# Kernel optimization log

Measured on AMD Instinct MI355X. Metric: run time of the kernel, lower is better.

## Reference

```python
import jax, jax.numpy as jnp
import numpy as np

N = 100000
E = 1600000
F_IN = 64
ACT = 8
NEG_SLOPE = 0.2


def _p(key, shape, scale=0.1):
    return jax.random.normal(key, shape, dtype=jnp.float32) * scale


def setup_inputs() -> dict:
    key = jax.random.key(0)
    ks = jax.random.split(key, 20)
    x = jax.random.normal(ks[0], (N, F_IN), dtype=jnp.float32)
    edge_index = jax.random.randint(ks[1], (2, E), 0, N, dtype=jnp.int64)
    edge_attr = jax.random.normal(ks[2], (E, 2), dtype=jnp.float32)
    # conv1: in=64, heads=4, out=16 -> 64
    H1, C1 = 4, 16
    Wl1 = _p(ks[3], (F_IN, H1 * C1)); bl1 = jnp.zeros((H1 * C1,), jnp.float32)
    Wr1 = _p(ks[4], (F_IN, H1 * C1)); br1 = jnp.zeros((H1 * C1,), jnp.float32)
    We1 = _p(ks[5], (2, H1 * C1))
    att1 = _p(ks[6], (H1, C1))
    b1 = jnp.zeros((H1 * C1,), jnp.float32)
    # conv2: in=64, heads=2, out=32 -> 64
    H2, C2 = 2, 32
    Wl2 = _p(ks[7], (H1 * C1, H2 * C2)); bl2 = jnp.zeros((H2 * C2,), jnp.float32)
    Wr2 = _p(ks[8], (H1 * C1, H2 * C2)); br2 = jnp.zeros((H2 * C2,), jnp.float32)
    We2 = _p(ks[9], (2, H2 * C2))
    att2 = _p(ks[10], (H2, C2))
    b2 = jnp.zeros((H2 * C2,), jnp.float32)
    Wm = _p(ks[11], (H2 * C2, ACT)); bm = jnp.zeros((ACT,), jnp.float32)
    return dict(x=x, edge_index=edge_index, edge_attr=edge_attr,
                Wl1=Wl1, bl1=bl1, Wr1=Wr1, br1=br1, We1=We1, att1=att1, b1=b1,
                Wl2=Wl2, bl2=bl2, Wr2=Wr2, br2=br2, We2=We2, att2=att2, b2=b2,
                Wm=Wm, bm=bm)


def gatv2_layer(x, src, dst, ea, Wl, bl, Wr, br, We, att, b, n_nodes, heads, ch):
    """PyG GATv2Conv with concat=True, add_self_loops=True (fill_value='mean')."""
    # self loops: edge attr = mean of incoming edge attrs per node (0 if none)
    deg = jax.ops.segment_sum(jnp.ones((src.shape[0],), ea.dtype), dst, n_nodes)
    loop_attr = jax.ops.segment_sum(ea, dst, n_nodes) / jnp.maximum(deg, 1.0)[:, None]
    loop = jnp.arange(n_nodes, dtype=src.dtype)
    s = jnp.concatenate([src, loop]); d = jnp.concatenate([dst, loop])
    ea_full = jnp.concatenate([ea, loop_attr], axis=0)
    xl = (x @ Wl + bl).reshape(n_nodes, heads, ch)   # source transform
    xr = (x @ Wr + br).reshape(n_nodes, heads, ch)   # target transform
    ee = (ea_full @ We).reshape(-1, heads, ch)
    e = jax.nn.leaky_relu(xl[s] + xr[d] + ee, NEG_SLOPE)  # [E', H, C]
    logits = jnp.einsum('ehc,hc->eh', e, att)             # [E', H]
    # segment softmax over destination (every node has a self loop -> non-empty)
    m = jax.ops.segment_max(logits, d, n_nodes)
    expl = jnp.exp(logits - m[d])
    denom = jax.ops.segment_sum(expl, d, n_nodes)
    alpha = expl / (denom[d] + 1e-16)
    out = jax.ops.segment_sum(xl[s] * alpha[:, :, None], d, n_nodes)
    return out.reshape(n_nodes, heads * ch) + b


def reference(x, edge_index, edge_attr, Wl1, bl1, Wr1, br1, We1, att1, b1,
              Wl2, bl2, Wr2, br2, We2, att2, b2, Wm, bm):
    src, dst = edge_index[0], edge_index[1]
    h = jax.nn.relu(gatv2_layer(x, src, dst, edge_attr, Wl1, bl1, Wr1, br1,
                                We1, att1, b1, N, 4, 16))
    h = jax.nn.relu(gatv2_layer(h, src, dst, edge_attr, Wl2, bl2, Wr2, br2,
                                We2, att2, b2, N, 2, 32))
    return jnp.tanh(h @ Wm + bm)
```

## Files before the change

kernel.cpp:

```cpp
#include <hip/hip_runtime.h>
#include <hip/hip_bf16.h>


constexpr int CAP = 64;

typedef float v2f __attribute__((ext_vector_type(2)));

static __device__ __forceinline__ float bf2f(__hip_bfloat16 v) { return __bfloat162float(v); }
static __device__ __forceinline__ float bits2f(unsigned int u) { return __uint_as_float(u << 16); }
static __device__ __forceinline__ unsigned int f2bfbits(float f) {
  unsigned int u = __float_as_uint(f);
  return ((u + 0x7FFFu + ((u >> 16) & 1u)) >> 16) & 0xFFFFu;
}
static __device__ __forceinline__ float bcast(float v, int k) {
  return __int_as_float(__builtin_amdgcn_readlane(__float_as_int(v), k));
}

template <int CTRL>
static __device__ __forceinline__ float dpp_add(float v) {
  int m = __builtin_amdgcn_update_dpp(0, __float_as_int(v), CTRL, 0xf, 0xf, false);
  return v + __int_as_float(m);
}
static __device__ __forceinline__ float row16_sum(float p) {
  p = dpp_add<0x128>(p);
  p = dpp_add<0x124>(p);
  p = dpp_add<0x122>(p);
  p = dpp_add<0x121>(p);
  return p;
}
static __device__ __forceinline__ float quad_sum(float p) {
  p = dpp_add<0xB1>(p);
  p = dpp_add<0x4E>(p);
  return p;
}
static __device__ __forceinline__ float wave64_sum(float p) {
  p = row16_sum(p);
  p += __shfl_xor(p, 16);
  p += __shfl_xor(p, 32);
  return p;
}

template <typename T> static __device__ __forceinline__ float ldv(const T* p, size_t i);
template <> __device__ __forceinline__ float ldv<float>(const float* p, size_t i) { return p[i]; }
template <> __device__ __forceinline__ float ldv<__hip_bfloat16>(const __hip_bfloat16* p, size_t i) {
  return bf2f(p[i]);
}
template <typename T> static __device__ __forceinline__ void stv(T* p, size_t i, float v);
template <> __device__ __forceinline__ void stv<float>(float* p, size_t i, float v) { p[i] = v; }
template <> __device__ __forceinline__ void stv<__hip_bfloat16>(__hip_bfloat16* p, size_t i,
                                                                float v) {
  p[i] = __float2bfloat16(v);
}

__global__ void k_count(const int* __restrict__ dst, int* __restrict__ cnt, int E, int N) {
  int i = blockIdx.x * 256 + threadIdx.x;
  if (i >= E) return;
  int d = dst[i]; d = min(max(d, 0), N - 1);
  atomicAdd(&cnt[d], 1);
}

__global__ __launch_bounds__(1024) void k_scan_local(const int* __restrict__ deg,
                                                     int* __restrict__ off,
                                                     int* __restrict__ bsum, int n) {
  __shared__ int s[1024];
  int t = threadIdx.x;
  int g = blockIdx.x * 1024 + t;
  int v = (g < n) ? deg[g] : 0;
  s[t] = v;
  __syncthreads();
  for (int o = 1; o < 1024; o <<= 1) {
    int add = (t >= o) ? s[t - o] : 0;
    __syncthreads();
    s[t] += add;
    __syncthreads();
  }
  if (g < n) off[g] = s[t] - v;
  if (t == 1023) bsum[blockIdx.x] = s[t];
}

__global__ __launch_bounds__(256) void k_scan_part(const int* __restrict__ bsum,
                                                   int* __restrict__ boff,
                                                   int* __restrict__ off, int nb, int n) {
  __shared__ int s[256];
  int t = threadIdx.x;
  int v = (t < nb) ? bsum[t] : 0;
  s[t] = v;
  __syncthreads();
  for (int o = 1; o < 256; o <<= 1) {
    int add = (t >= o) ? s[t - o] : 0;
    __syncthreads();
    s[t] += add;
    __syncthreads();
  }
  if (t < nb) boff[t] = s[t] - v;
  if (t == nb - 1) off[n] = s[t];
}

__global__ __launch_bounds__(1024) void k_scan_add(int* __restrict__ off, int* __restrict__ cursor,
                                                   const int* __restrict__ boff, int n) {
  int g = blockIdx.x * 1024 + threadIdx.x;
  if (g < n) {
    int v = off[g] + boff[blockIdx.x];
    off[g] = v;
    cursor[g] = v;
  }
}

__global__ void k_scatter_x(const int* __restrict__ src, const int* __restrict__ dst,
                            const float* __restrict__ ea, int* __restrict__ cursor,
                            long long* __restrict__ csr, int E, int N) {
  const int group = blockIdx.x & 7;
  const int chunk = blockIdx.x >> 3;
  const int r0 = (int)(((long long)N * group) >> 3);
  const int r1 = (int)(((long long)N * (group + 1)) >> 3);
  int i0 = (chunk * 256 + threadIdx.x) * 4;
  if (i0 >= E) return;
  if (i0 + 4 <= E) {
    int4 sv = *(const int4*)(src + i0);
    int4 dv = *(const int4*)(dst + i0);
    float4 ea01 = *(const float4*)(ea + 2 * i0);
    float4 ea23 = *(const float4*)(ea + 2 * i0 + 4);
    int ss[4] = {sv.x, sv.y, sv.z, sv.w};
    int dd[4] = {dv.x, dv.y, dv.z, dv.w};
    float e0[4] = {ea01.x, ea01.z, ea23.x, ea23.z};
    float e1[4] = {ea01.y, ea01.w, ea23.y, ea23.w};
#pragma unroll
    for (int j = 0; j < 4; ++j) {
      int d = min(max(dd[j], 0), N - 1);
      if (d >= r0 && d < r1) {
        int s = min(max(ss[j], 0), N - 1);
        unsigned int ep = f2bfbits(e0[j]) | (f2bfbits(e1[j]) << 16);
        long long rec = (long long)(unsigned int)s | ((long long)ep << 32);
        int slot = atomicAdd(&cursor[d], 1);
        if (slot < CAP) csr[(long long)d * CAP + slot] = rec;
      }
    }
  } else {
    for (int i = i0; i < E; ++i) {
      int d = min(max(dst[i], 0), N - 1);
      if (d >= r0 && d < r1) {
        int s = min(max(src[i], 0), N - 1);
        unsigned int ep = f2bfbits(ea[2 * i]) | (f2bfbits(ea[2 * i + 1]) << 16);
        long long rec = (long long)(unsigned int)s | ((long long)ep << 32);
        int slot = atomicAdd(&cursor[d], 1);
        if (slot < CAP) csr[(long long)d * CAP + slot] = rec;
      }
    }
  }
}

__global__ void k_scatter_d(const int* __restrict__ src, const int* __restrict__ dst,
                            const float* __restrict__ ea, int* __restrict__ cursor,
                            long long* __restrict__ csr, int E, int N) {
  int i = blockIdx.x * 256 + threadIdx.x;
  if (i >= E) return;
  int d = min(max(dst[i], 0), N - 1);
  int s = min(max(src[i], 0), N - 1);
  unsigned int ep = f2bfbits(ea[2 * i]) | (f2bfbits(ea[2 * i + 1]) << 16);
  long long rec = (long long)(unsigned int)s | ((long long)ep << 32);
  int slot = atomicAdd(&cursor[d], 1);
  csr[slot] = rec;
}

__global__ __launch_bounds__(256) void k_gemm_xlxr(const float* __restrict__ in,
                                                   const float* __restrict__ Wl,
                                                   const float* __restrict__ bl,
                                                   const float* __restrict__ Wr,
                                                   const float* __restrict__ br,
                                                   unsigned short* __restrict__ xlb,
                                                   float* __restrict__ xr, int n) {
  int lane = threadIdx.x & 63, wave = threadIdx.x >> 6;
  float wl[64], wr[64];
#pragma unroll
  for (int k = 0; k < 64; ++k) {
    wl[k] = Wl[k * 64 + lane];
    wr[k] = Wr[k * 64 + lane];
  }
  float blc = bl[lane], brc = br[lane];
  const int stride = gridDim.x * 4;
  int node = blockIdx.x * 4 + wave;
  if (node >= n) return;
  float xv = in[(size_t)node * 64 + lane];
  while (node < n) {
    int nxt = node + stride;
    float xn = (nxt < n) ? in[(size_t)nxt * 64 + lane] : 0.f;
    float accl = blc, accr = brc;
#pragma unroll
    for (int k = 0; k < 64; ++k) {
      float s = bcast(xv, k);
      accl = fmaf(s, wl[k], accl);
      accr = fmaf(s, wr[k], accr);
    }
    xlb[(size_t)node * 64 + lane] = (unsigned short)f2bfbits(accl);
    xr[(size_t)node * 64 + lane] = accr;
    node = nxt;
    xv = xn;
  }
}

template <int C, bool FUSE_MLP>
__global__ __launch_bounds__(256) void k_agg4p(const unsigned short* __restrict__ xlb,
                                               const float* __restrict__ xr,
                                               const long long* __restrict__ csr,
                                               const int* __restrict__ cnt,
                                               const float* __restrict__ We,
                                               const float* __restrict__ att,
                                               const float* __restrict__ b,
                                               const float* __restrict__ Wm,
                                               const float* __restrict__ bm,
                                               float* __restrict__ hout,
                                               float* __restrict__ fout, int n) {
  __shared__ long long smeta[4][CAP];
  const int lane = threadIdx.x & 63;
  const int wv = threadIdx.x >> 6;
  const int sub = lane & 15;
  const int grp = lane >> 4;

  float4 t4;
  t4 = ((const float4*)We)[sub];        const v2f We0a = {t4.x, t4.y}, We0b = {t4.z, t4.w};
  t4 = ((const float4*)(We + 64))[sub]; const v2f We1a = {t4.x, t4.y}, We1b = {t4.z, t4.w};
  t4 = ((const float4*)att)[sub];       const v2f atta = {t4.x, t4.y}, attb = {t4.z, t4.w};
  t4 = ((const float4*)b)[sub];         const v2f ba = {t4.x, t4.y},  bb = {t4.z, t4.w};

  const int wstride = gridDim.x * 4;
  for (int wid = blockIdx.x * 4 + wv; wid < n; wid += wstride) {
    const int node = __builtin_amdgcn_readfirstlane(wid);
    float4 x4 = ((const float4*)(xr + (size_t)node * 64))[sub];
    const v2f xra = {x4.x, x4.y}, xrb = {x4.z, x4.w};
    uint2 xself = ((const uint2*)xlb)[((unsigned)node << 4) + sub];

    int dg = cnt[node];
    int c64 = min(dg, CAP);
    long long meta = (lane < c64) ? __builtin_nontemporal_load(&csr[(size_t)node * CAP + lane])
                                  : 0LL;
    smeta[wv][lane] = meta;
    int mhi = (int)((unsigned long long)meta >> 32);
    float ea0acc = __uint_as_float((unsigned)mhi << 16);
    float ea1acc = __uint_as_float((unsigned)mhi & 0xffff0000u);

    float den = 0.f;
    v2f numa = {0.f, 0.f}, numb = {0.f, 0.f};

    int iters = (c64 + 3) >> 2;
    long long m0 = smeta[wv][grp];
    uint2 xg0 = ((const uint2*)xlb)[(((unsigned)(unsigned int)m0) << 4) + sub];
    for (int t = 0; t < iters; ++t) {
      long long m1 = 0;
      uint2 xg1 = {0u, 0u};
      if (t + 1 < iters) {
        m1 = smeta[wv][(t + 1) * 4 + grp];
        xg1 = ((const uint2*)xlb)[(((unsigned)(unsigned int)m1) << 4) + sub];
      }
      unsigned epc = (unsigned)((unsigned long long)m0 >> 32);
      float ea0 = __uint_as_float(epc << 16);
      float ea1 = __uint_as_float(epc & 0xffff0000u);
      v2f ea0v = {ea0, ea0}, ea1v = {ea1, ea1};
      v2f xca = {__uint_as_float(xg0.x << 16), __uint_as_float(xg0.x & 0xffff0000u)};
      v2f xcb = {__uint_as_float(xg0.y << 16), __uint_as_float(xg0.y & 0xffff0000u)};
      v2f eA = __builtin_elementwise_fma(We1a, ea1v,
               __builtin_elementwise_fma(We0a, ea0v, xca + xra));
      v2f eB = __builtin_elementwise_fma(We1b, ea1v,
               __builtin_elementwise_fma(We0b, ea0v, xcb + xrb));
      eA = __builtin_elementwise_max(eA, eA * 0.2f);
      eB = __builtin_elementwise_max(eB, eB * 0.2f);
      v2f pv = __builtin_elementwise_fma(eB, attb, eA * atta);
      float p = pv.x + pv.y;
      p = quad_sum(p);
      if (C == 32) p = dpp_add<0x141>(p);
      bool valid = ((t << 2) + grp) < c64;
      float ex = valid ? __expf(p) : 0.f;
      v2f exv = {ex, ex};
      den += ex;
      numa = __builtin_elementwise_fma(exv, xca, numa);
      numb = __builtin_elementwise_fma(exv, xcb, numb);
      m0 = m1;
      xg0 = xg1;
    }

    den += __shfl_xor(den, 16);
    den += __shfl_xor(den, 32);
    numa.x += __shfl_xor(numa.x, 16); numa.x += __shfl_xor(numa.x, 32);
    numa.y += __shfl_xor(numa.y, 16); numa.y += __shfl_xor(numa.y, 32);
    numb.x += __shfl_xor(numb.x, 16); numb.x += __shfl_xor(numb.x, 32);
    numb.y += __shfl_xor(numb.y, 16); numb.y += __shfl_xor(numb.y, 32);

    v2f xsa = {__uint_as_float(xself.x << 16), __uint_as_float(xself.x & 0xffff0000u)};
    v2f xsb = {__uint_as_float(xself.y << 16), __uint_as_float(xself.y & 0xffff0000u)};
    {
      float s0 = wave64_sum(ea0acc);
      float s1 = wave64_sum(ea1acc);
      float inv = 1.0f / (float)max(dg, 1);
      v2f a0v = {s0 * inv, s0 * inv}, a1v = {s1 * inv, s1 * inv};
      v2f eA = __builtin_elementwise_fma(We1a, a1v,
               __builtin_elementwise_fma(We0a, a0v, xsa + xra));
      v2f eB = __builtin_elementwise_fma(We1b, a1v,
               __builtin_elementwise_fma(We0b, a0v, xsb + xrb));
      eA = __builtin_elementwise_max(eA, eA * 0.2f);
      eB = __builtin_elementwise_max(eB, eB * 0.2f);
      v2f pv = __builtin_elementwise_fma(eB, attb, eA * atta);
      float p = quad_sum(pv.x + pv.y);
      if (C == 32) p = dpp_add<0x141>(p);
      float ex = __expf(p);
      v2f exv = {ex, ex};
      den += ex;
      numa = __builtin_elementwise_fma(exv, xsa, numa);
      numb = __builtin_elementwise_fma(exv, xsb, numb);
    }

    float inv = 1.0f / (den + 1e-16f);
    v2f invv = {inv, inv};
    v2f oa = __builtin_elementwise_max(__builtin_elementwise_fma(numa, invv, ba), (v2f){0.f, 0.f});
    v2f ob = __builtin_elementwise_max(__builtin_elementwise_fma(numb, invv, bb), (v2f){0.f, 0.f});

    if (!FUSE_MLP) {
      if (grp == 0) {
        float4 o4 = {oa.x, oa.y, ob.x, ob.y};
        ((float4*)(hout + (size_t)node * 64))[sub] = o4;
      }
    } else {
      float mine = 0.f;
#pragma unroll
      for (int j = 0; j < 8; ++j) {
        float p = oa.x * Wm[(4 * sub + 0) * 8 + j];
        p = fmaf(oa.y, Wm[(4 * sub + 1) * 8 + j], p);
        p = fmaf(ob.x, Wm[(4 * sub + 2) * 8 + j], p);
        p = fmaf(ob.y, Wm[(4 * sub + 3) * 8 + j], p);
        p = row16_sum(p);
        if (lane == j) mine = p;
      }
      if (lane < 8) fout[(size_t)node * 8 + lane] = tanhf(mine + bm[lane]);
    }
  }
}

template <int C, bool FUSE_MLP>
__global__ __launch_bounds__(256) void k_agg4d(const unsigned short* __restrict__ xlb,
                                               const float* __restrict__ xr,
                                               const long long* __restrict__ csr,
                                               const int* __restrict__ off,
                                               const float* __restrict__ We,
                                               const float* __restrict__ att,
                                               const float* __restrict__ b,
                                               const float* __restrict__ Wm,
                                               const float* __restrict__ bm,
                                               float* __restrict__ hout,
                                               float* __restrict__ fout, int n) {
  const int lane = threadIdx.x & 63;
  const int sub = lane & 15;
  const int grp = lane >> 4;
  const int grp4 = grp << 2;
  const float4 We04 = ((const float4*)We)[sub];
  const float4 We14 = ((const float4*)(We + 64))[sub];
  const float4 att4 = ((const float4*)att)[sub];
  const float4 b4 = ((const float4*)b)[sub];

  const int wstride = gridDim.x * 4;
  for (int wid = blockIdx.x * 4 + (threadIdx.x >> 6); wid < n; wid += wstride) {
    const int node = __builtin_amdgcn_readfirstlane(wid);
    float4 xr4 = ((const float4*)(xr + (size_t)node * 64))[sub];
    uint2 xself = ((const uint2*)xlb)[((unsigned)node << 4) + sub];
    int start = off[node], end = off[node + 1], dg = end - start;
    float den = 0.f;
    float4 num = {0.f, 0.f, 0.f, 0.f};
    float ea0acc = 0.f, ea1acc = 0.f;
    for (int base = start; base < end; base += 64) {
      int c64 = min(64, end - base);
      long long meta = (lane < c64) ? __builtin_nontemporal_load(&csr[base + lane]) : 0LL;
      int mlo = (int)(unsigned long long)meta;
      int mhi = (int)((unsigned long long)meta >> 32);
      ea0acc += __uint_as_float((unsigned)mhi << 16);
      ea1acc += __uint_as_float((unsigned)mhi & 0xffff0000u);
      int iters = (c64 + 3) >> 2;
      int se0 = __builtin_amdgcn_ds_bpermute(grp4, mlo);
      int ep0 = __builtin_amdgcn_ds_bpermute(grp4, mhi);
      uint2 xg0 = ((const uint2*)xlb)[((unsigned)se0 << 4) + sub];
      for (int t = 0; t < iters; ++t) {
        int ep1 = 0;
        uint2 xg1 = {0u, 0u};
        if (t + 1 < iters) {
          int idx = ((t + 1) << 4) + grp4;
          int se1 = __builtin_amdgcn_ds_bpermute(idx, mlo);
          ep1 = __builtin_amdgcn_ds_bpermute(idx, mhi);
          xg1 = ((const uint2*)xlb)[((unsigned)se1 << 4) + sub];
        }
        float4 xc;
        xc.x = __uint_as_float(xg0.x << 16);
        xc.y = __uint_as_float(xg0.x & 0xffff0000u);
        xc.z = __uint_as_float(xg0.y << 16);
        xc.w = __uint_as_float(xg0.y & 0xffff0000u);
        unsigned epc = (unsigned)ep0;
        float ea0 = __uint_as_float(epc << 16);
        float ea1 = __uint_as_float(epc & 0xffff0000u);
        float4 e;
        e.x = fmaf(ea1, We14.x, fmaf(ea0, We04.x, xc.x + xr4.x));
        e.y = fmaf(ea1, We14.y, fmaf(ea0, We04.y, xc.y + xr4.y));
        e.z = fmaf(ea1, We14.z, fmaf(ea0, We04.z, xc.z + xr4.z));
        e.w = fmaf(ea1, We14.w, fmaf(ea0, We04.w, xc.w + xr4.w));
        e.x = fmaxf(e.x, 0.2f * e.x);
        e.y = fmaxf(e.y, 0.2f * e.y);
        e.z = fmaxf(e.z, 0.2f * e.z);
        e.w = fmaxf(e.w, 0.2f * e.w);
        float p = e.x * att4.x;
        p = fmaf(e.y, att4.y, p);
        p = fmaf(e.z, att4.z, p);
        p = fmaf(e.w, att4.w, p);
        p = quad_sum(p);
        if (C == 32) p = dpp_add<0x141>(p);
        bool valid = ((t << 2) + grp) < c64;
        float ex = valid ? __expf(p) : 0.f;
        den += ex;
        num.x = fmaf(ex, xc.x, num.x);
        num.y = fmaf(ex, xc.y, num.y);
        num.z = fmaf(ex, xc.z, num.z);
        num.w = fmaf(ex, xc.w, num.w);
        ep0 = ep1;
        xg0 = xg1;
      }
    }
    den += __shfl_xor(den, 16);
    den += __shfl_xor(den, 32);
    num.x += __shfl_xor(num.x, 16); num.x += __shfl_xor(num.x, 32);
    num.y += __shfl_xor(num.y, 16); num.y += __shfl_xor(num.y, 32);
    num.z += __shfl_xor(num.z, 16); num.z += __shfl_xor(num.z, 32);
    num.w += __shfl_xor(num.w, 16); num.w += __shfl_xor(num.w, 32);
    float4 xls4;
    xls4.x = __uint_as_float(xself.x << 16);
    xls4.y = __uint_as_float(xself.x & 0xffff0000u);
    xls4.z = __uint_as_float(xself.y << 16);
    xls4.w = __uint_as_float(xself.y & 0xffff0000u);
    {
      float s0 = wave64_sum(ea0acc);
      float s1 = wave64_sum(ea1acc);
      float inv = 1.0f / (float)max(dg, 1);
      float a0 = s0 * inv, a1 = s1 * inv;
      float4 e;
      e.x = fmaf(a1, We14.x, fmaf(a0, We04.x, xls4.x + xr4.x));
      e.y = fmaf(a1, We14.y, fmaf(a0, We04.y, xls4.y + xr4.y));
      e.z = fmaf(a1, We14.z, fmaf(a0, We04.z, xls4.z + xr4.z));
      e.w = fmaf(a1, We14.w, fmaf(a0, We04.w, xls4.w + xr4.w));
      e.x = fmaxf(e.x, 0.2f * e.x);
      e.y = fmaxf(e.y, 0.2f * e.y);
      e.z = fmaxf(e.z, 0.2f * e.z);
      e.w = fmaxf(e.w, 0.2f * e.w);
      float p = e.x * att4.x;
      p = fmaf(e.y, att4.y, p);
      p = fmaf(e.z, att4.z, p);
      p = fmaf(e.w, att4.w, p);
      p = quad_sum(p);
      if (C == 32) p = dpp_add<0x141>(p);
      float ex = __expf(p);
      den += ex;
      num.x = fmaf(ex, xls4.x, num.x);
      num.y = fmaf(ex, xls4.y, num.y);
      num.z = fmaf(ex, xls4.z, num.z);
      num.w = fmaf(ex, xls4.w, num.w);
    }
    float inv = 1.0f / (den + 1e-16f);
    float4 o;
    o.x = fmaxf(fmaf(num.x, inv, b4.x), 0.f);
    o.y = fmaxf(fmaf(num.y, inv, b4.y), 0.f);
    o.z = fmaxf(fmaf(num.z, inv, b4.z), 0.f);
    o.w = fmaxf(fmaf(num.w, inv, b4.w), 0.f);
    if (!FUSE_MLP) {
      if (grp == 0) ((float4*)(hout + (size_t)node * 64))[sub] = o;
    } else {
      float mine = 0.f;
#pragma unroll
      for (int j = 0; j < 8; ++j) {
        float p = o.x * Wm[(4 * sub + 0) * 8 + j];
        p = fmaf(o.y, Wm[(4 * sub + 1) * 8 + j], p);
        p = fmaf(o.z, Wm[(4 * sub + 2) * 8 + j], p);
        p = fmaf(o.w, Wm[(4 * sub + 3) * 8 + j], p);
        p = row16_sum(p);
        if (lane == j) mine = p;
      }
      if (lane < 8) fout[(size_t)node * 8 + lane] = tanhf(mine + bm[lane]);
    }
  }
}

template <typename TIN, typename TOUT>
__global__ __launch_bounds__(256) void k_gemm_gen(const TIN* __restrict__ in,
                                                  const float* __restrict__ Wl,
                                                  const float* __restrict__ bl,
                                                  const float* __restrict__ Wr,
                                                  const float* __restrict__ br,
                                                  TOUT* __restrict__ xl, TOUT* __restrict__ xr,
                                                  int n) {
  int lane = threadIdx.x & 63, wave = threadIdx.x >> 6;
  float wl[64], wr[64];
#pragma unroll
  for (int k = 0; k < 64; ++k) {
    wl[k] = Wl[k * 64 + lane];
    wr[k] = Wr[k * 64 + lane];
  }
  float blc = bl[lane], brc = br[lane];
  for (int node = blockIdx.x * 4 + wave; node < n; node += gridDim.x * 4) {
    float xv = ldv(in, (size_t)node * 64 + lane);
    float accl = blc, accr = brc;
#pragma unroll
    for (int k = 0; k < 64; ++k) {
      float s = bcast(xv, k);
      accl = fmaf(s, wl[k], accl);
      accr = fmaf(s, wr[k], accr);
    }
    stv(xl, (size_t)node * 64 + lane, accl);
    stv(xr, (size_t)node * 64 + lane, accr);
  }
}

template <int C, bool FUSE_MLP, typename ST>
__global__ __launch_bounds__(256) void k_agg(const ST* __restrict__ xl, const ST* __restrict__ xr,
                                             const long long* __restrict__ csr,
                                             const int* __restrict__ off,
                                             const float* __restrict__ We,
                                             const float* __restrict__ att,
                                             const float* __restrict__ b,
                                             const float* __restrict__ Wm,
                                             const float* __restrict__ bm, ST* __restrict__ hout,
                                             float* __restrict__ fout, int n) {
  int wid = (int)((blockIdx.x * blockDim.x + threadIdx.x) >> 6);
  int lane = threadIdx.x & 63;
  if (wid >= n) return;
  const int node = __builtin_amdgcn_readfirstlane(wid);
  float xr_c = ldv(xr, (size_t)node * 64 + lane);
  float xl_self = ldv(xl, (size_t)node * 64 + lane);
  float We0 = We[lane], We1 = We[64 + lane], attc = att[lane], bc = b[lane];
  int start = off[node], end = off[node + 1], dg = end - start;
  float den = 0.f, num = 0.f, ea0acc = 0.f, ea1acc = 0.f;
  for (int base = start; base < end; base += 64) {
    int c64 = min(64, end - base);
    long long meta = (lane < c64) ? csr[base + lane] : 0;
    int mlo = (int)(unsigned long long)meta;
    int mhi = (int)((unsigned long long)meta >> 32);
    ea0acc += bits2f((unsigned)mhi & 0xffffu);
    ea1acc += bits2f((unsigned)mhi >> 16);
    for (int t = 0; t < c64; ++t) {
      int s = __builtin_amdgcn_readlane(mlo, t);
      unsigned ep = (unsigned)__builtin_amdgcn_readlane(mhi, t);
      float xls = ldv(xl, (size_t)s * 64 + lane);
      float e = xls + xr_c + bits2f(ep & 0xffffu) * We0 + bits2f(ep >> 16) * We1;
      e = fmaxf(e, 0.2f * e);
      float p = row16_sum(e * attc);
      if (C == 32) p += __shfl_xor(p, 16);
      float ex = __expf(p);
      den += ex;
      num = fmaf(ex, xls, num);
    }
  }
  {
    float s0 = wave64_sum(ea0acc), s1 = wave64_sum(ea1acc);
    float inv = 1.0f / (float)max(dg, 1);
    float e = xl_self + xr_c + s0 * inv * We0 + s1 * inv * We1;
    e = fmaxf(e, 0.2f * e);
    float p = row16_sum(e * attc);
    if (C == 32) p += __shfl_xor(p, 16);
    float ex = __expf(p);
    den += ex;
    num = fmaf(ex, xl_self, num);
  }
  float o = fmaxf(num / (den + 1e-16f) + bc, 0.f);
  if (!FUSE_MLP) {
    stv(hout, (size_t)node * 64 + lane, o);
  } else {
    float mine = 0.f;
#pragma unroll
    for (int j = 0; j < 8; ++j) {
      float p = wave64_sum(o * Wm[lane * 8 + j]);
      if (lane == j) mine = p;
    }
    if (lane < 8) fout[(size_t)node * 8 + lane] = tanhf(mine + bm[lane]);
  }
}

extern "C" void kernel_launch(void* const* d_in, const int* in_sizes, int n_in,
                              void* d_out, int out_size, void* d_ws, size_t ws_size,
                              hipStream_t stream) {
  const float* x = (const float*)d_in[0];
  const int* ei = (const int*)d_in[1];
  const float* ea = (const float*)d_in[2];
  const float* Wl1 = (const float*)d_in[3];
  const float* bl1 = (const float*)d_in[4];
  const float* Wr1 = (const float*)d_in[5];
  const float* br1 = (const float*)d_in[6];
  const float* We1 = (const float*)d_in[7];
  const float* att1 = (const float*)d_in[8];
  const float* b1 = (const float*)d_in[9];
  const float* Wl2 = (const float*)d_in[10];
  const float* bl2 = (const float*)d_in[11];
  const float* Wr2 = (const float*)d_in[12];
  const float* br2 = (const float*)d_in[13];
  const float* We2 = (const float*)d_in[14];
  const float* att2 = (const float*)d_in[15];
  const float* b2 = (const float*)d_in[16];
  const float* Wm = (const float*)d_in[17];
  const float* bm = (const float*)d_in[18];
  float* out = (float*)d_out;

  const int N = in_sizes[0] / 64;
  const int E = in_sizes[1] / 2;
  const int* src = ei;
  const int* dst = ei + E;

  auto al = [](size_t x) { return (x + 255) & ~(size_t)255; };
  const size_t needA = al((size_t)N * 4) + al((size_t)N * CAP * 8) + al((size_t)N * 64 * 2) +
                       al((size_t)N * 64 * 4) + al((size_t)N * 64 * 4);
  const size_t fixedB = al((size_t)N * 4) + al((size_t)(N + 1) * 4) + al((size_t)N * 4) +
                        al(1024) + al(1024) + al((size_t)E * 8);
  const size_t needB = fixedB + al((size_t)N * 64 * 2) + 2 * al((size_t)N * 64 * 4);

  char* p = (char*)d_ws;
  auto alloc = [&](size_t bytes) {
    char* r = p;
    p += (bytes + 255) & ~(size_t)255;
    return r;
  };

  const int egrid4 = (E + 1023) / 1024;
  const int egrid = (E + 255) / 256;
  const int agrid = 2048;
  const int ggrid = 1024;
  const int NB = (N + 1023) / 1024;

  if (ws_size >= needA) {
    int* cnt = (int*)alloc((size_t)N * 4);
    long long* csr = (long long*)alloc((size_t)N * CAP * 8);
    unsigned short* xlb = (unsigned short*)alloc((size_t)N * 64 * 2);
    float* xr = (float*)alloc((size_t)N * 64 * 4);
    float* h = (float*)alloc((size_t)N * 64 * 4);

    hipMemsetAsync(cnt, 0, (size_t)N * 4, stream);
    k_scatter_x<<<egrid4 * 8, 256, 0, stream>>>(src, dst, ea, cnt, csr, E, N);

    k_gemm_xlxr<<<ggrid, 256, 0, stream>>>(x, Wl1, bl1, Wr1, br1, xlb, xr, N);
    k_agg4p<16, false><<<agrid, 256, 0, stream>>>(xlb, xr, csr, cnt, We1, att1, b1, nullptr,
                                                  nullptr, h, nullptr, N);
    k_gemm_xlxr<<<ggrid, 256, 0, stream>>>(h, Wl2, bl2, Wr2, br2, xlb, xr, N);
    k_agg4p<32, true><<<agrid, 256, 0, stream>>>(xlb, xr, csr, cnt, We2, att2, b2, Wm, bm,
                                                 nullptr, out, N);
  } else if (ws_size >= needB) {
    int* cnt = (int*)alloc((size_t)N * 4);
    int* off = (int*)alloc((size_t)(N + 1) * 4);
    int* cursor = (int*)alloc((size_t)N * 4);
    int* bsum = (int*)alloc(1024);
    int* boff = (int*)alloc(1024);
    long long* csr = (long long*)alloc((size_t)E * 8);
    unsigned short* xlb = (unsigned short*)alloc((size_t)N * 64 * 2);
    float* xr = (float*)alloc((size_t)N * 64 * 4);
    float* h = (float*)alloc((size_t)N * 64 * 4);

    hipMemsetAsync(cnt, 0, (size_t)N * 4, stream);
    k_count<<<egrid, 256, 0, stream>>>(dst, cnt, E, N);
    k_scan_local<<<NB, 1024, 0, stream>>>(cnt, off, bsum, N);
    k_scan_part<<<1, 256, 0, stream>>>(bsum, boff, off, NB, N);
    k_scan_add<<<NB, 1024, 0, stream>>>(off, cursor, boff, N);
    k_scatter_d<<<egrid, 256, 0, stream>>>(src, dst, ea, cursor, csr, E, N);

    k_gemm_xlxr<<<ggrid, 256, 0, stream>>>(x, Wl1, bl1, Wr1, br1, xlb, xr, N);
    k_agg4d<16, false><<<agrid, 256, 0, stream>>>(xlb, xr, csr, off, We1, att1, b1, nullptr,
                                                  nullptr, h, nullptr, N);
    k_gemm_xlxr<<<ggrid, 256, 0, stream>>>(h, Wl2, bl2, Wr2, br2, xlb, xr, N);
    k_agg4d<32, true><<<agrid, 256, 0, stream>>>(xlb, xr, csr, off, We2, att2, b2, Wm, bm,
                                                 nullptr, out, N);
  } else {
    int* cnt = (int*)alloc((size_t)N * 4);
    int* off = (int*)alloc((size_t)(N + 1) * 4);
    int* cursor = (int*)alloc((size_t)N * 4);
    int* bsum = (int*)alloc(1024);
    int* boff = (int*)alloc(1024);
    long long* csr = (long long*)alloc((size_t)E * 8);
    __hip_bfloat16* xl = (__hip_bfloat16*)alloc((size_t)N * 64 * 2);
    __hip_bfloat16* xr = (__hip_bfloat16*)alloc((size_t)N * 64 * 2);
    __hip_bfloat16* h = (__hip_bfloat16*)alloc((size_t)N * 64 * 2);

    hipMemsetAsync(cnt, 0, (size_t)N * 4, stream);
    k_count<<<egrid, 256, 0, stream>>>(dst, cnt, E, N);
    k_scan_local<<<NB, 1024, 0, stream>>>(cnt, off, bsum, N);
    k_scan_part<<<1, 256, 0, stream>>>(bsum, boff, off, NB, N);
    k_scan_add<<<NB, 1024, 0, stream>>>(off, cursor, boff, N);
    k_scatter_d<<<egrid, 256, 0, stream>>>(src, dst, ea, cursor, csr, E, N);

    k_gemm_gen<float, __hip_bfloat16><<<ggrid, 256, 0, stream>>>(x, Wl1, bl1, Wr1, br1, xl, xr, N);
    k_agg<16, false, __hip_bfloat16><<<(N + 3) / 4, 256, 0, stream>>>(
        xl, xr, csr, off, We1, att1, b1, nullptr, nullptr, h, nullptr, N);
    k_gemm_gen<__hip_bfloat16, __hip_bfloat16><<<ggrid, 256, 0, stream>>>(h, Wl2, bl2, Wr2, br2,
                                                                          xl, xr, N);
    k_agg<32, true, __hip_bfloat16><<<(N + 3) / 4, 256, 0, stream>>>(
        xl, xr, csr, off, We2, att2, b2, Wm, bm, nullptr, out, N);
  }
}
```

Baseline: 450.9 us.

## Process eight edges per wave iteration in GATv2 aggregation with 8-lane groups

Reworks the aggregation kernel so each wave handles eight neighbor edges per iteration instead of four. Each edge is covered by 8 lanes loading 16-byte bf16 chunks rather than 16 lanes loading 8 bytes, which halves the loop trip count and widens the gather loads. Head reductions move to smaller DPP patterns, and the cross-group reductions and the fused MLP are adapted to the new lane layout. In exchange each lane holds more registers and does more arithmetic, and low-degree nodes leave more lanes idle.

After: 470.7 us. +4.4%, slower.

```diff
diff --git a/kernel.cpp b/kernel.cpp
--- a/kernel.cpp
+++ b/kernel.cpp
@@ -28,16 +28,38 @@
   p = dpp_add<0x121>(p);
   return p;
 }
-static __device__ __forceinline__ float quad_sum(float p) {
-  p = dpp_add<0xB1>(p);
-  p = dpp_add<0x4E>(p);
-  return p;
-}
 static __device__ __forceinline__ float wave64_sum(float p) {
   p = row16_sum(p);
   p += __shfl_xor(p, 16);
   p += __shfl_xor(p, 32);
   return p;
+}
+static __device__ __forceinline__ float grp_sum(float v) {
+  v = dpp_add<0x128>(v);
+  v += __shfl_xor(v, 16);
+  v += __shfl_xor(v, 32);
+  return v;
+}
+static __device__ __forceinline__ float sub8_sum(float v) {
+  v = dpp_add<0x124>(v);
+  v = dpp_add<0x122>(v);
+  v = dpp_add<0x121>(v);
+  return v;
+}
+
+static __device__ __forceinline__ void unpack8(uint4 g, v2f* r) {
+  r[0] = (v2f){__uint_as_float(g.x << 16), __uint_as_float(g.x & 0xffff0000u)};
+  r[1] = (v2f){__uint_as_float(g.y << 16), __uint_as_float(g.y & 0xffff0000u)};
+  r[2] = (v2f){__uint_as_float(g.z << 16), __uint_as_float(g.z & 0xffff0000u)};
+  r[3] = (v2f){__uint_as_float(g.w << 16), __uint_as_float(g.w & 0xffff0000u)};
+}
+static __device__ __forceinline__ void load8(const float* p, int sub, v2f* r) {
+  float4 u = ((const float4*)p)[2 * sub];
+  float4 v = ((const float4*)p)[2 * sub + 1];
+  r[0] = (v2f){u.x, u.y};
+  r[1] = (v2f){u.z, u.w};
+  r[2] = (v2f){v.x, v.y};
+  r[3] = (v2f){v.z, v.w};
 }
 
 template <typename T> static __device__ __forceinline__ float ldv(const T* p, size_t i);
@@ -199,7 +221,7 @@
 }
 
 template <int C, bool FUSE_MLP>
-__global__ __launch_bounds__(256) void k_agg4p(const unsigned short* __restrict__ xlb,
+__global__ __launch_bounds__(256) void k_agg8p(const unsigned short* __restrict__ xlb,
                                                const float* __restrict__ xr,
                                                const long long* __restrict__ csr,
                                                const int* __restrict__ cnt,
@@ -213,21 +235,20 @@
   __shared__ long long smeta[4][CAP];
   const int lane = threadIdx.x & 63;
   const int wv = threadIdx.x >> 6;
-  const int sub = lane & 15;
-  const int grp = lane >> 4;
-
-  float4 t4;
-  t4 = ((const float4*)We)[sub];        const v2f We0a = {t4.x, t4.y}, We0b = {t4.z, t4.w};
-  t4 = ((const float4*)(We + 64))[sub]; const v2f We1a = {t4.x, t4.y}, We1b = {t4.z, t4.w};
-  t4 = ((const float4*)att)[sub];       const v2f atta = {t4.x, t4.y}, attb = {t4.z, t4.w};
-  t4 = ((const float4*)b)[sub];         const v2f ba = {t4.x, t4.y},  bb = {t4.z, t4.w};
+  const int sub = lane & 7;
+  const int grp = lane >> 3;
+
+  v2f We0[4], We1[4], attv[4];
+  load8(We, sub, We0);
+  load8(We + 64, sub, We1);
+  load8(att, sub, attv);
 
   const int wstride = gridDim.x * 4;
   for (int wid = blockIdx.x * 4 + wv; wid < n; wid += wstride) {
     const int node = __builtin_amdgcn_readfirstlane(wid);
-    float4 x4 = ((const float4*)(xr + (size_t)node * 64))[sub];
-    const v2f xra = {x4.x, x4.y}, xrb = {x4.z, x4.w};
-    uint2 xself = ((const uint2*)xlb)[((unsigned)node << 4) + sub];
+    v2f xrv[4];
+    load8(xr + (size_t)node * 64, sub, xrv);
+    uint4 xself = ((const uint4*)xlb)[((unsigned)node << 3) + sub];
 
     int dg = cnt[node];
     int c64 = min(dg, CAP);
@@ -239,93 +260,103 @@
     float ea1acc = __uint_as_float((unsigned)mhi & 0xffff0000u);
 
     float den = 0.f;
-    v2f numa = {0.f, 0.f}, numb = {0.f, 0.f};
-
-    int iters = (c64 + 3) >> 2;
+    v2f num[4] = {{0.f, 0.f}, {0.f, 0.f}, {0.f, 0.f}, {0.f, 0.f}};
+
+    int iters = (c64 + 7) >> 3;
     long long m0 = smeta[wv][grp];
-    uint2 xg0 = ((const uint2*)xlb)[(((unsigned)(unsigned int)m0) << 4) + sub];
+    uint4 xg0 = ((const uint4*)xlb)[(((unsigned)(unsigned int)m0) << 3) + sub];
     for (int t = 0; t < iters; ++t) {
       long long m1 = 0;
-      uint2 xg1 = {0u, 0u};
+      uint4 xg1 = {0u, 0u, 0u, 0u};
       if (t + 1 < iters) {
-        m1 = smeta[wv][(t + 1) * 4 + grp];
-        xg1 = ((const uint2*)xlb)[(((unsigned)(unsigned int)m1) << 4) + sub];
+        m1 = smeta[wv][(t + 1) * 8 + grp];
+        xg1 = ((const uint4*)xlb)[(((unsigned)(unsigned int)m1) << 3) + sub];
       }
       unsigned epc = (unsigned)((unsigned long long)m0 >> 32);
-      float ea0 = __uint_as_float(epc << 16);
-      float ea1 = __uint_as_float(epc & 0xffff0000u);
-      v2f ea0v = {ea0, ea0}, ea1v = {ea1, ea1};
-      v2f xca = {__uint_as_float(xg0.x << 16), __uint_as_float(xg0.x & 0xffff0000u)};
-      v2f xcb = {__uint_as_float(xg0.y << 16), __uint_as_float(xg0.y & 0xffff0000u)};
-      v2f eA = __builtin_elementwise_fma(We1a, ea1v,
-               __builtin_elementwise_fma(We0a, ea0v, xca + xra));
-      v2f eB = __builtin_elementwise_fma(We1b, ea1v,
-               __builtin_elementwise_fma(We0b, ea0v, xcb + xrb));
-      eA = __builtin_elementwise_max(eA, eA * 0.2f);
-      eB = __builtin_elementwise_max(eB, eB * 0.2f);
-      v2f pv = __builtin_elementwise_fma(eB, attb, eA * atta);
+      v2f ea0v = {__uint_as_float(epc << 16), __uint_as_float(epc << 16)};
+      v2f ea1v = {__uint_as_float(epc & 0xffff0000u), __uint_as_float(epc & 0xffff0000u)};
+      v2f xc[4];
+      unpack8(xg0, xc);
+      v2f pv;
+#pragma unroll
+      for (int q = 0; q < 4; ++q) {
+        v2f e = __builtin_elementwise_fma(We1[q], ea1v,
+                __builtin_elementwise_fma(We0[q], ea0v, xc[q] + xrv[q]));
+        e = __builtin_elementwise_max(e, e * 0.2f);
+        pv = (q == 0) ? e * attv[0] : __builtin_elementwise_fma(e, attv[q], pv);
+      }
       float p = pv.x + pv.y;
-      p = quad_sum(p);
-      if (C == 32) p = dpp_add<0x141>(p);
-      bool valid = ((t << 2) + grp) < c64;
+      p = dpp_add<0xB1>(p);
+      if (C == 32) p = dpp_add<0x4E>(p);
+      bool valid = (t * 8 + grp) < c64;
       float ex = valid ? __expf(p) : 0.f;
       v2f exv = {ex, ex};
       den += ex;
-      numa = __builtin_elementwise_fma(exv, xca, numa);
-      numb = __builtin_elementwise_fma(exv, xcb, numb);
+#pragma unroll
+      for (int q = 0; q < 4; ++q) num[q] = __builtin_elementwise_fma(exv, xc[q], num[q]);
       m0 = m1;
       xg0 = xg1;
     }
 
-    den += __shfl_xor(den, 16);
-    den += __shfl_xor(den, 32);
-    numa.x += __shfl_xor(numa.x, 16); numa.x += __shfl_xor(numa.x, 32);
-    numa.y += __shfl_xor(numa.y, 16); numa.y += __shfl_xor(numa.y, 32);
-    numb.x += __shfl_xor(numb.x, 16); numb.x += __shfl_xor(numb.x, 32);
-    numb.y += __shfl_xor(numb.y, 16); numb.y += __shfl_xor(numb.y, 32);
-
-    v2f xsa = {__uint_as_float(xself.x << 16), __uint_as_float(xself.x & 0xffff0000u)};
-    v2f xsb = {__uint_as_float(xself.y << 16), __uint_as_float(xself.y & 0xffff0000u)};
+    den = grp_sum(den);
+#pragma unroll
+    for (int q = 0; q < 4; ++q) {
+      num[q].x = grp_sum(num[q].x);
+      num[q].y = grp_sum(num[q].y);
+    }
+
+    v2f xs[4];
+    unpack8(xself, xs);
     {
       float s0 = wave64_sum(ea0acc);
       float s1 = wave64_sum(ea1acc);
-      float inv = 1.0f / (float)max(dg, 1);
-      v2f a0v = {s0 * inv, s0 * inv}, a1v = {s1 * inv, s1 * inv};
-      v2f eA = __builtin_elementwise_fma(We1a, a1v,
-               __builtin_elementwise_fma(We0a, a0v, xsa + xra));
-      v2f eB = __builtin_elementwise_fma(We1b, a1v,
-               __builtin_elementwise_fma(We0b, a0v, xsb + xrb));
-      eA = __builtin_elementwise_max(eA, eA * 0.2f);
-      eB = __builtin_elementwise_max(eB, eB * 0.2f);
-      v2f pv = __builtin_elementwise_fma(eB, attb, eA * atta);
-      float p = quad_sum(pv.x + pv.y);
-      if (C == 32) p = dpp_add<0x141>(p);
+      float minv = 1.0f / (float)max(dg, 1);
+      v2f a0v = {s0 * minv, s0 * minv}, a1v = {s1 * minv, s1 * minv};
+      v2f pv;
+#pragma unroll
+      for (int q = 0; q < 4; ++q) {
+        v2f e = __builtin_elementwise_fma(We1[q], a1v,
+                __builtin_elementwise_fma(We0[q], a0v, xs[q] + xrv[q]));
+        e = __builtin_elementwise_max(e, e * 0.2f);
+        pv = (q == 0) ? e * attv[0] : __builtin_elementwise_fma(e, attv[q], pv);
+      }
+      float p = pv.x + pv.y;
+      p = dpp_add<0xB1>(p);
+      if (C == 32) p = dpp_add<0x4E>(p);
       float ex = __expf(p);
       v2f exv = {ex, ex};
       den += ex;
-      numa = __builtin_elementwise_fma(exv, xsa, numa);
-      numb = __builtin_elementwise_fma(exv, xsb, numb);
-    }
-
-    float inv = 1.0f / (den + 1e-16f);
-    v2f invv = {inv, inv};
-    v2f oa = __builtin_elementwise_max(__builtin_elementwise_fma(numa, invv, ba), (v2f){0.f, 0.f});
-    v2f ob = __builtin_elementwise_max(__builtin_elementwise_fma(numb, invv, bb), (v2f){0.f, 0.f});
+#pragma unroll
+      for (int q = 0; q < 4; ++q) num[q] = __builtin_elementwise_fma(exv, xs[q], num[q]);
+    }
+
+    float invd = 1.0f / (den + 1e-16f);
+    v2f invv = {invd, invd};
+    v2f bv[4];
+    load8(b, sub, bv);
+    v2f o[4];
+#pragma unroll
+    for (int q = 0; q < 4; ++q)
+      o[q] = __builtin_elementwise_max(__builtin_elementwise_fma(num[q], invv, bv[q]),
+                                       (v2f){0.f, 0.f});
 
     if (!FUSE_MLP) {
       if (grp == 0) {
-        float4 o4 = {oa.x, oa.y, ob.x, ob.y};
-        ((float4*)(hout + (size_t)node * 64))[sub] = o4;
+        float4 oA = {o[0].x, o[0].y, o[1].x, o[1].y};
+        float4 oB = {o[2].x, o[2].y, o[3].x, o[3].y};
+        ((float4*)(hout + (size_t)node * 64))[2 * sub] = oA;
+        ((float4*)(hout + (size_t)node * 64))[2 * sub + 1] = oB;
       }
     } else {
+      const float* wmrow = Wm + (8 * sub) * 8;
+      float oc[8] = {o[0].x, o[0].y, o[1].x, o[1].y, o[2].x, o[2].y, o[3].x, o[3].y};
       float mine = 0.f;
 #pragma unroll
       for (int j = 0; j < 8; ++j) {
-        float p = oa.x * Wm[(4 * sub + 0) * 8 + j];
-        p = fmaf(oa.y, Wm[(4 * sub + 1) * 8 + j], p);
-        p = fmaf(ob.x, Wm[(4 * sub + 2) * 8 + j], p);
-        p = fmaf(ob.y, Wm[(4 * sub + 3) * 8 + j], p);
-        p = row16_sum(p);
+        float p = oc[0] * wmrow[j];
+#pragma unroll
+        for (int k = 1; k < 8; ++k) p = fmaf(oc[k], wmrow[k * 8 + j], p);
+        p = sub8_sum(p);
         if (lane == j) mine = p;
       }
       if (lane < 8) fout[(size_t)node * 8 + lane] = tanhf(mine + bm[lane]);
@@ -404,7 +435,8 @@
         p = fmaf(e.y, att4.y, p);
         p = fmaf(e.z, att4.z, p);
         p = fmaf(e.w, att4.w, p);
-        p = quad_sum(p);
+        p = dpp_add<0xB1>(p);
+        p = dpp_add<0x4E>(p);
         if (C == 32) p = dpp_add<0x141>(p);
         bool valid = ((t << 2) + grp) < c64;
         float ex = valid ? __expf(p) : 0.f;
@@ -446,7 +478,8 @@
       p = fmaf(e.y, att4.y, p);
       p = fmaf(e.z, att4.z, p);
       p = fmaf(e.w, att4.w, p);
-      p = quad_sum(p);
+      p = dpp_add<0xB1>(p);
+      p = dpp_add<0x4E>(p);
       if (C == 32) p = dpp_add<0x141>(p);
       float ex = __expf(p);
       den += ex;
@@ -633,10 +666,10 @@
     k_scatter_x<<<egrid4 * 8, 256, 0, stream>>>(src, dst, ea, cnt, csr, E, N);
 
     k_gemm_xlxr<<<ggrid, 256, 0, stream>>>(x, Wl1, bl1, Wr1, br1, xlb, xr, N);
-    k_agg4p<16, false><<<agrid, 256, 0, stream>>>(xlb, xr, csr, cnt, We1, att1, b1, nullptr,
+    k_agg8p<16, false><<<agrid, 256, 0, stream>>>(xlb, xr, csr, cnt, We1, att1, b1, nullptr,
                                                   nullptr, h, nullptr, N);
     k_gemm_xlxr<<<ggrid, 256, 0, stream>>>(h, Wl2, bl2, Wr2, br2, xlb, xr, N);
-    k_agg4p<32, true><<<agrid, 256, 0, stream>>>(xlb, xr, csr, cnt, We2, att2, b2, Wm, bm,
+    k_agg8p<32, true><<<agrid, 256, 0, stream>>>(xlb, xr, csr, cnt, We2, att2, b2, Wm, bm,
                                                  nullptr, out, N);
   } else if (ws_size >= needB) {
     int* cnt = (int*)alloc((size_t)N * 4);
```

## Replace 8-pass edge scatter with two-pass destination-range partition then scatter

Applied to the files above, without the earlier changes.

Before this, CSR build launched the scatter kernel over eight destination-range groups, so every group re-read all edges and filtered them. It now runs a partition kernel that reads each edge once, bins it into one of eight destination-range buckets using a shared histogram and a global cursor, and also zeroes the count array. A second kernel then scatters each bucket into the per-node CSR slots with atomics. This cuts the repeated edge reads and the memset, at the cost of an extra intermediate buffer write and read. It only runs when the workspace is large enough.

After: 472.5 us. 4.8% more time.

```diff
diff --git a/kernel.cpp b/kernel.cpp
--- a/kernel.cpp
+++ b/kernel.cpp
@@ -103,6 +103,94 @@
     int v = off[g] + boff[blockIdx.x];
     off[g] = v;
     cursor[g] = v;
+  }
+}
+
+__global__ __launch_bounds__(256) void k_part(const int* __restrict__ src,
+                                              const int* __restrict__ dst,
+                                              const float* __restrict__ ea,
+                                              long long* __restrict__ prec,
+                                              int* __restrict__ pdst,
+                                              int* __restrict__ gcur,
+                                              int* __restrict__ cnt,
+                                              int E, int N, int ecap) {
+  __shared__ int hist[8], base[8], pos[8];
+  const int gid = blockIdx.x * 256 + threadIdx.x;
+  if (gid < N) cnt[gid] = 0;
+  if (threadIdx.x < 8) {
+    hist[threadIdx.x] = 0;
+    pos[threadIdx.x] = 0;
+  }
+  __syncthreads();
+
+  const int i0 = gid * 4;
+  int myg[4], dd[4];
+  long long rec[4];
+  bool have[4] = {false, false, false, false};
+  if (i0 + 4 <= E) {
+    int4 sv = *(const int4*)(src + i0);
+    int4 dv = *(const int4*)(dst + i0);
+    float4 ea01 = *(const float4*)(ea + 2 * i0);
+    float4 ea23 = *(const float4*)(ea + 2 * i0 + 4);
+    int ss[4] = {sv.x, sv.y, sv.z, sv.w};
+    int dr[4] = {dv.x, dv.y, dv.z, dv.w};
+    float e0[4] = {ea01.x, ea01.z, ea23.x, ea23.z};
+    float e1[4] = {ea01.y, ea01.w, ea23.y, ea23.w};
+#pragma unroll
+    for (int j = 0; j < 4; ++j) {
+      int d = min(max(dr[j], 0), N - 1);
+      int s = min(max(ss[j], 0), N - 1);
+      unsigned ep = f2bfbits(e0[j]) | (f2bfbits(e1[j]) << 16);
+      dd[j] = d;
+      rec[j] = (long long)(unsigned int)s | ((long long)ep << 32);
+      myg[j] = (int)(((long long)d * 8) / N);
+      have[j] = true;
+      atomicAdd(&hist[myg[j]], 1);
+    }
+  } else if (i0 < E) {
+    for (int j = 0; i0 + j < E; ++j) {
+      int d = min(max(dst[i0 + j], 0), N - 1);
+      int s = min(max(src[i0 + j], 0), N - 1);
+      unsigned ep = f2bfbits(ea[2 * (i0 + j)]) | (f2bfbits(ea[2 * (i0 + j) + 1]) << 16);
+      dd[j] = d;
+      rec[j] = (long long)(unsigned int)s | ((long long)ep << 32);
+      myg[j] = (int)(((long long)d * 8) / N);
+      have[j] = true;
+      atomicAdd(&hist[myg[j]], 1);
+    }
+  }
+  __syncthreads();
+  if (threadIdx.x < 8 && hist[threadIdx.x] > 0)
+    base[threadIdx.x] = atomicAdd(&gcur[threadIdx.x], hist[threadIdx.x]);
+  __syncthreads();
+#pragma unroll
+  for (int j = 0; j < 4; ++j) {
+    if (have[j]) {
+      int g = myg[j];
+      int r = atomicAdd(&pos[g], 1);
+      size_t idx = (size_t)g * ecap + base[g] + r;
+      prec[idx] = rec[j];
+      pdst[idx] = dd[j];
+    }
+  }
+}
+
+__global__ __launch_bounds__(256) void k_scat2(const long long* __restrict__ prec,
+                                               const int* __restrict__ pdst,
+                                               const int* __restrict__ gcur,
+                                               int* __restrict__ cnt,
+                                               long long* __restrict__ csr, int ecap) {
+  const int g = blockIdx.x & 7;
+  const int chunk = blockIdx.x >> 3;
+  const int cg = gcur[g];
+  const long long* pr = prec + (size_t)g * ecap;
+  const int* pd = pdst + (size_t)g * ecap;
+  const int stride = (gridDim.x >> 3) * 256;
+  for (int i = chunk * 256 + threadIdx.x; i < cg; i += stride) {
+    long long rec = pr[i];
+    int d = pd[i];
+    int slot = atomicAdd(&cnt[d], 1);
+    if (slot < CAP) csr[(long long)d * CAP + slot] = rec;
   }
 }
 
@@ -603,8 +691,10 @@
   const int* dst = ei + E;
 
   auto al = [](size_t x) { return (x + 255) & ~(size_t)255; };
+  const int ecap = E / 8 + 32768;
   const size_t needA = al((size_t)N * 4) + al((size_t)N * CAP * 8) + al((size_t)N * 64 * 2) +
                        al((size_t)N * 64 * 4) + al((size_t)N * 64 * 4);
+  const size_t need2P = needA + al((size_t)ecap * 8 * 8) + al((size_t)ecap * 8 * 4) + al(64);
   const size_t fixedB = al((size_t)N * 4) + al((size_t)(N + 1) * 4) + al((size_t)N * 4) +
                         al(1024) + al(1024) + al((size_t)E * 8);
   const size_t needB = fixedB + al((size_t)N * 64 * 2) + 2 * al((size_t)N * 64 * 4);
@@ -629,8 +719,18 @@
     float* xr = (float*)alloc((size_t)N * 64 * 4);
     float* h = (float*)alloc((size_t)N * 64 * 4);
 
-    hipMemsetAsync(cnt, 0, (size_t)N * 4, stream);
-    k_scatter_x<<<egrid4 * 8, 256, 0, stream>>>(src, dst, ea, cnt, csr, E, N);
+    if (ws_size >= need2P) {
+      long long* prec = (long long*)alloc((size_t)ecap * 8 * 8);
+      int* pdst = (int*)alloc((size_t)ecap * 8 * 4);
+      int* gcur = (int*)alloc(64);
+      hipMemsetAsync(gcur, 0, 64, stream);
+      int pgrid = egrid4 > (N + 255) / 256 ? egrid4 : (N + 255) / 256;
+      k_part<<<pgrid, 256, 0, stream>>>(src, dst, ea, prec, pdst, gcur, cnt, E, N, ecap);
+      k_scat2<<<6400, 256, 0, stream>>>(prec, pdst, gcur, cnt, csr, ecap);
+    } else {
+      hipMemsetAsync(cnt, 0, (size_t)N * 4, stream);
+      k_scatter_x<<<egrid4 * 8, 256, 0, stream>>>(src, dst, ea, cnt, csr, E, N);
+    }
 
     k_gemm_xlxr<<<ggrid, 256, 0, stream>>>(x, Wl1, bl1, Wr1, br1, xlb, xr, N);
     k_agg4p<16, false><<<agrid, 256, 0, stream>>>(xlb, xr, csr, cnt, We1, att1, b1, nullptr,
```
